# Kernel optimization log

Hardware: AMD Instinct MI355X
Metric: run time of the kernel (lower is better)

## Reference

```python
import jax, jax.numpy as jnp
import numpy as np

B, L, H, D, EF = 2, 2048, 16, 64, 4
HID = H * D            # 1024
QKVP = HID * (3 + EF)  # 7168
VP = HID * (1 + EF)    # 5120
LN_EPS = 1e-5


def layer_norm(x, g, b):
    m = jnp.mean(x, axis=-1, keepdims=True)
    v = jnp.mean(jnp.square(x - m), axis=-1, keepdims=True)
    return (x - m) * jax.lax.rsqrt(v + LN_EPS) * g + b


def shift_seq(x, n):
    # shift along seq (axis -2) by n, zero-padding the front (matches F.pad (0,0,n,-n))
    return jnp.pad(x, ((0, 0), (n, 0), (0, 0)))[:, :-n, :]


def setup_inputs() -> dict:
    key = jax.random.key(0)
    ks = jax.random.split(key, 4)
    x = jax.random.normal(ks[0], (B, L, HID), dtype=jnp.float32)
    W_in = jax.random.normal(ks[1], (QKVP, HID), dtype=jnp.float32) * (HID ** -0.5)
    W_out = jax.random.normal(ks[2], (HID, VP), dtype=jnp.float32) * (VP ** -0.5)
    slopes = (2.0 ** jnp.linspace(0.0, -6.0, H)).astype(jnp.float32)
    return {
        "x": x,
        "in_ln_g": jnp.ones((HID,), jnp.float32),
        "in_ln_b": jnp.zeros((HID,), jnp.float32),
        "W_in": W_in,
        "mid_ln_g": jnp.ones((QKVP,), jnp.float32),
        "mid_ln_b": jnp.zeros((QKVP,), jnp.float32),
        "slopes": slopes,
        "W_out": W_out,
        "out_ln_g": jnp.ones((HID,), jnp.float32),
        "out_ln_b": jnp.zeros((HID,), jnp.float32),
    }


def reference(x, in_ln_g, in_ln_b, W_in, mid_ln_g, mid_ln_b, slopes, W_out, out_ln_g, out_ln_b):
    b, l, d = x.shape
    d8 = d // 8
    x = layer_norm(x, in_ln_g, in_ln_b)
    # in-place torch shifts compose: ch [0,d/8) shifted by 1; ch [d/8,d/4) shifted by 1 then 2 (=3)
    x = jnp.concatenate([
        shift_seq(x[..., :d8], 1),
        shift_seq(x[..., d8:2 * d8], 3),
        x[..., 2 * d8:],
    ], axis=-1)
    h = layer_norm(jax.nn.relu(jnp.einsum('bld,od->blo', x, W_in)), mid_ln_g, mid_ln_b)
    q = h[..., :HID].reshape(b, l, H, D)
    k = h[..., HID:2 * HID].reshape(b, l, H, D)
    v = h[..., 2 * HID:3 * HID].reshape(b, l, H, D)
    p = h[..., 3 * HID:]  # [b, l, HID*EF]
    scores = jnp.einsum('bihd,bjhd->bhij', q, k) * (D ** -0.5)
    causal = jnp.where(jnp.tril(jnp.ones((l, l), dtype=bool)), 0.0, -1e10).astype(scores.dtype)
    alibi = jnp.arange(l, dtype=scores.dtype)[None, None, None, :] * slopes[None, :, None, None]
    a = jax.nn.softmax(scores + causal[None, None] + alibi, axis=-1)
    o = jnp.einsum('bhij,bjhd->bihd', a, v).reshape(b, l, HID)
    pg = jax.nn.gelu(p, approximate=False) * jnp.roll(p, 1, axis=-1)
    out = jnp.einsum('blv,dv->bld', jnp.concatenate([o, pg], axis=-1), W_out)
    return layer_norm(out, out_ln_g, out_ln_b)
```

## Files before the change

### kernel.cpp

```cpp
#include <hip/hip_runtime.h>
#include <math.h>

#define L_SEQ 2048
#define NB 2
#define NH 16
#define HID 1024
#define QKVP 7168
#define VP 5120
#define NROWS 4096
#define LN_EPS 1e-5f

typedef unsigned short u16;
using s16x4 = __attribute__((ext_vector_type(4))) short;
using s16x8 = __attribute__((ext_vector_type(8))) short;
using f32x4 = __attribute__((ext_vector_type(4))) float;

__device__ __forceinline__ u16 f2bf(float f) {
  unsigned u = __float_as_uint(f);
  u += 0x7FFFu + ((u >> 16) & 1u);
  return (u16)(u >> 16);
}
__device__ __forceinline__ float bf2f(u16 h) {
  return __uint_as_float((unsigned)h << 16);
}
struct HiLo { short hi, lo; };
__device__ __forceinline__ HiLo split2(float x) {
  HiLo r;
  const u16 h = f2bf(x);
  r.hi = (short)h;
  r.lo = (short)f2bf(x - bf2f(h));
  return r;
}
__device__ __forceinline__ void split4(float4 v, s16x4& h4, s16x4& l4) {
  const HiLo a = split2(v.x), b = split2(v.y), c = split2(v.z), d = split2(v.w);
  h4[0] = a.hi; l4[0] = a.lo;
  h4[1] = b.hi; l4[1] = b.lo;
  h4[2] = c.hi; l4[2] = c.lo;
  h4[3] = d.hi; l4[3] = d.lo;
}
__device__ __forceinline__ void split4v(f32x4 v, s16x4& h4, s16x4& l4) {
  const HiLo a = split2(v[0]), b = split2(v[1]), c = split2(v[2]), d = split2(v[3]);
  h4[0] = a.hi; l4[0] = a.lo;
  h4[1] = b.hi; l4[1] = b.lo;
  h4[2] = c.hi; l4[2] = c.lo;
  h4[3] = d.hi; l4[3] = d.lo;
}
__device__ __forceinline__ s16x8 shuf8(s16x4 a, s16x4 b) {
  return __builtin_shufflevector(a, b, 0, 1, 2, 3, 4, 5, 6, 7);
}

__device__ __forceinline__ float blk_sum256(float v, float* sm) {
#pragma unroll
  for (int m = 32; m >= 1; m >>= 1) v += __shfl_xor(v, m, 64);
  __syncthreads();
  if ((threadIdx.x & 63) == 0) sm[threadIdx.x >> 6] = v;
  __syncthreads();
  return sm[0] + sm[1] + sm[2] + sm[3];
}

__global__ __launch_bounds__(256) void ln_shift_kernel(
    const float* __restrict__ x, const float* __restrict__ g,
    const float* __restrict__ bb, float* __restrict__ xs) {
  __shared__ float sm[4];
  const int row = blockIdx.x;
  const int l = row & (L_SEQ - 1);
  const int t = threadIdx.x;
  const float4 v = reinterpret_cast<const float4*>(x + (size_t)row * HID)[t];
  float s = v.x + v.y + v.z + v.w;
  const float mean = blk_sum256(s, sm) * (1.0f / HID);
  const float dx = v.x - mean, dy = v.y - mean, dz = v.z - mean, dw = v.w - mean;
  const float sq = dx * dx + dy * dy + dz * dz + dw * dw;
  const float var = blk_sum256(sq, sm) * (1.0f / HID);
  const float rstd = rsqrtf(var + LN_EPS);
  const float4 gv = reinterpret_cast<const float4*>(g)[t];
  const float4 bv = reinterpret_cast<const float4*>(bb)[t];
  float4 n;
  n.x = dx * rstd * gv.x + bv.x;
  n.y = dy * rstd * gv.y + bv.y;
  n.z = dz * rstd * gv.z + bv.z;
  n.w = dw * rstd * gv.w + bv.w;
  const int c0 = t * 4;
  const float4 zero = make_float4(0.f, 0.f, 0.f, 0.f);
  if (c0 < 128) {
    if (l + 1 < L_SEQ) reinterpret_cast<float4*>(xs + (size_t)(row + 1) * HID)[t] = n;
    if (l == 0)        reinterpret_cast<float4*>(xs + (size_t)row * HID)[t] = zero;
  } else if (c0 < 256) {
    if (l + 3 < L_SEQ) reinterpret_cast<float4*>(xs + (size_t)(row + 3) * HID)[t] = n;
    if (l < 3)         reinterpret_cast<float4*>(xs + (size_t)row * HID)[t] = zero;
  } else {
    reinterpret_cast<float4*>(xs + (size_t)row * HID)[t] = n;
  }
}

template <bool RELU, bool A_REMAP>
__global__ __launch_bounds__(256, 2) void gemm_f32_hilo(
    const float* __restrict__ A, const float* __restrict__ Bw,
    float* __restrict__ C, int N, int K, int lda, int nbx) {
  __shared__ __align__(16) u16 Ah[128][40];
  __shared__ __align__(16) u16 Al[128][40];
  __shared__ __align__(16) u16 Bh[128][40];
  __shared__ __align__(16) u16 Bl[128][40];

  const int cpx = (int)gridDim.x >> 3;
  const int b0 = blockIdx.x;
  const int swz = (b0 & 7) * cpx + (b0 >> 3);
  const int bx = swz % nbx, by = swz / nbx;
  const int m0 = by * 128, n0 = bx * 128;

  const int t = threadIdx.x;
  const int lane = t & 63, w = t >> 6;
  const int wr = (w >> 1) * 64, wc = (w & 1) * 64;
  const int lrow = lane & 15;
  const int lkg = (lane >> 4) * 4;

  f32x4 acc[4][4] = {};

  const int sr = t >> 1;
  const int sk = (t & 1) * 16;

  for (int k0 = 0; k0 < K; k0 += 32) {
    int ak = sk + k0;
    if (A_REMAP && ak >= 1024) ak += 2048;
    const float* ap = A + (size_t)(m0 + sr) * lda + ak;
    const float* bp = Bw + (size_t)(n0 + sr) * K + sk + k0;
    const float4 av0 = *(const float4*)(ap);
    const float4 av1 = *(const float4*)(ap + 4);
    const float4 av2 = *(const float4*)(ap + 8);
    const float4 av3 = *(const float4*)(ap + 12);
    const float4 bv0 = *(const float4*)(bp);
    const float4 bv1 = *(const float4*)(bp + 4);
    const float4 bv2 = *(const float4*)(bp + 8);
    const float4 bv3 = *(const float4*)(bp + 12);
    __syncthreads();
    {
      s16x4 h0, l0, h1, l1;
      split4(av0, h0, l0); split4(av1, h1, l1);
      *(s16x8*)&Ah[sr][sk] = shuf8(h0, h1);
      *(s16x8*)&Al[sr][sk] = shuf8(l0, l1);
      split4(av2, h0, l0); split4(av3, h1, l1);
      *(s16x8*)&Ah[sr][sk + 8] = shuf8(h0, h1);
      *(s16x8*)&Al[sr][sk + 8] = shuf8(l0, l1);
      split4(bv0, h0, l0); split4(bv1, h1, l1);
      *(s16x8*)&Bh[sr][sk] = shuf8(h0, h1);
      *(s16x8*)&Bl[sr][sk] = shuf8(l0, l1);
      split4(bv2, h0, l0); split4(bv3, h1, l1);
      *(s16x8*)&Bh[sr][sk + 8] = shuf8(h0, h1);
      *(s16x8*)&Bl[sr][sk + 8] = shuf8(l0, l1);
    }
    __syncthreads();

    s16x8 afh[4], afl[4], bfh[4], bfl[4];
#pragma unroll
    for (int f = 0; f < 4; ++f) {
      const int ar = wr + f * 16 + lrow;
      const int bc = wc + f * 16 + lrow;
      s16x4 p0, p1;
      p0 = *(const s16x4*)&Ah[ar][lkg]; p1 = *(const s16x4*)&Ah[ar][16 + lkg];
      afh[f] = shuf8(p0, p1);
      p0 = *(const s16x4*)&Al[ar][lkg]; p1 = *(const s16x4*)&Al[ar][16 + lkg];
      afl[f] = shuf8(p0, p1);
      p0 = *(const s16x4*)&Bh[bc][lkg]; p1 = *(const s16x4*)&Bh[bc][16 + lkg];
      bfh[f] = shuf8(p0, p1);
      p0 = *(const s16x4*)&Bl[bc][lkg]; p1 = *(const s16x4*)&Bl[bc][16 + lkg];
      bfl[f] = shuf8(p0, p1);
    }
#pragma unroll
    for (int i = 0; i < 4; ++i)
#pragma unroll
      for (int j = 0; j < 4; ++j) {
        acc[i][j] = __builtin_amdgcn_mfma_f32_16x16x32_bf16(afh[i], bfh[j], acc[i][j], 0, 0, 0);
        acc[i][j] = __builtin_amdgcn_mfma_f32_16x16x32_bf16(afh[i], bfl[j], acc[i][j], 0, 0, 0);
        acc[i][j] = __builtin_amdgcn_mfma_f32_16x16x32_bf16(afl[i], bfh[j], acc[i][j], 0, 0, 0);
      }
  }
#pragma unroll
  for (int i = 0; i < 4; ++i) {
    const int row0 = m0 + wr + i * 16 + lkg;
#pragma unroll
    for (int j = 0; j < 4; ++j) {
      const int col = n0 + wc + j * 16 + lrow;
#pragma unroll
      for (int r = 0; r < 4; ++r) {
        float v = acc[i][j][r];
        if (RELU) v = fmaxf(v, 0.f);
        C[(size_t)(row0 + r) * N + col] = v;
      }
    }
  }
}

__global__ __launch_bounds__(256) void mid_ln_kernel(
    float* __restrict__ h, const float* __restrict__ g, const float* __restrict__ bb) {
  __shared__ float sm[4];
  const int row = blockIdx.x;
  const int t = threadIdx.x;
  float* hr = h + (size_t)row * QKVP;
  float4 r[7];
  float s = 0.f;
#pragma unroll
  for (int j = 0; j < 7; ++j) {
    r[j] = reinterpret_cast<float4*>(hr)[t + j * 256];
    s += r[j].x + r[j].y + r[j].z + r[j].w;
  }
  const float mean = blk_sum256(s, sm) * (1.0f / QKVP);
  float sq = 0.f;
#pragma unroll
  for (int j = 0; j < 7; ++j) {
    r[j].x -= mean; r[j].y -= mean; r[j].z -= mean; r[j].w -= mean;
    sq += r[j].x * r[j].x + r[j].y * r[j].y + r[j].z * r[j].z + r[j].w * r[j].w;
  }
  const float rstd = rsqrtf(blk_sum256(sq, sm) * (1.0f / QKVP) + LN_EPS);
#pragma unroll
  for (int j = 0; j < 7; ++j) {
    const float4 gv = reinterpret_cast<const float4*>(g)[t + j * 256];
    const float4 bv = reinterpret_cast<const float4*>(bb)[t + j * 256];
    float4 o;
    o.x = r[j].x * rstd * gv.x + bv.x;
    o.y = r[j].y * rstd * gv.y + bv.y;
    o.z = r[j].z * rstd * gv.z + bv.z;
    o.w = r[j].w * rstd * gv.w + bv.w;
    reinterpret_cast<float4*>(hr)[t + j * 256] = o;
  }
}

__global__ __launch_bounds__(256) void attn_kernel(
    float* __restrict__ h, const float* __restrict__ slopes) {
  __shared__ __align__(16) u16 Kh[64][72];
  __shared__ __align__(16) u16 Kl[64][72];
  __shared__ __align__(16) u16 Vh[64][76];
  __shared__ __align__(16) u16 Vl[64][76];
  const int it = blockIdx.x, bh = blockIdx.y;
  const int b = bh >> 4, hh = bh & 15;
  const float slope = slopes[hh];
  const int t = threadIdx.x;
  const int lane = t & 63, w = t >> 6;
  const int li = lane & 15;
  const int g = lane >> 4;
  const int i0 = it * 64;
  const size_t base = (size_t)b * L_SEQ * QKVP;
  const int myrow = i0 + w * 16 + li;

  s16x8 qh[2], ql[2];
  {
    const float* qp = h + base + (size_t)myrow * QKVP + hh * 64 + 8 * g;
#pragma unroll
    for (int ks = 0; ks < 2; ++ks) {
      const float4 a0 = *(const float4*)(qp + 32 * ks);
      const float4 a1 = *(const float4*)(qp + 32 * ks + 4);
      s16x4 h0, l0, h1, l1;
      split4(a0, h0, l0);
      split4(a1, h1, l1);
      qh[ks] = shuf8(h0, h1);
      ql[ks] = shuf8(l0, l1);
    }
  }

  float m_run = -INFINITY, l_run = 0.f;
  f32x4 ot[4] = {};

  const int sj = t >> 2, sd = (t & 3) * 16;
  const int vj = (t >> 4) * 4, vd = (t & 15) * 4;
  const float* kbase = h + base + HID + hh * 64;
  const float* vbase = h + base + 2 * HID + hh * 64;

  for (int jt = 0; jt <= it; ++jt) {
    const int j0 = jt * 64;
    float4 kq[4], vq[4];
#pragma unroll
    for (int q = 0; q < 4; ++q)
      kq[q] = *(const float4*)(kbase + (size_t)(j0 + sj) * QKVP + sd + 4 * q);
#pragma unroll
    for (int r = 0; r < 4; ++r)
      vq[r] = *(const float4*)(vbase + (size_t)(j0 + vj + r) * QKVP + vd);
    __syncthreads();
    {
      s16x4 h0, l0, h1, l1;
      split4(kq[0], h0, l0); split4(kq[1], h1, l1);
      *(s16x8*)&Kh[sj][sd] = shuf8(h0, h1);
      *(s16x8*)&Kl[sj][sd] = shuf8(l0, l1);
      split4(kq[2], h0, l0); split4(kq[3], h1, l1);
      *(s16x8*)&Kh[sj][sd + 8] = shuf8(h0, h1);
      *(s16x8*)&Kl[sj][sd + 8] = shuf8(l0, l1);
    }
    {
      s16x4 vh4[4], vl4[4];
#pragma unroll
      for (int r = 0; r < 4; ++r) split4(vq[r], vh4[r], vl4[r]);
#pragma unroll
      for (int c = 0; c < 4; ++c) {
        s16x4 hc, lc;
#pragma unroll
        for (int r = 0; r < 4; ++r) { hc[r] = vh4[r][c]; lc[r] = vl4[r][c]; }
        *(s16x4*)&Vh[vd + c][vj] = hc;
        *(s16x4*)&Vl[vd + c][vj] = lc;
      }
    }
    __syncthreads();

    f32x4 sa[4] = {};
#pragma unroll
    for (int j4 = 0; j4 < 4; ++j4) {
      const int jr = j4 * 16 + li;
#pragma unroll
      for (int ks = 0; ks < 2; ++ks) {
        const s16x8 kh = *(const s16x8*)&Kh[jr][ks * 32 + 8 * g];
        const s16x8 kl = *(const s16x8*)&Kl[jr][ks * 32 + 8 * g];
        sa[j4] = __builtin_amdgcn_mfma_f32_16x16x32_bf16(kh, qh[ks], sa[j4], 0, 0, 0);
        sa[j4] = __builtin_amdgcn_mfma_f32_16x16x32_bf16(kh, ql[ks], sa[j4], 0, 0, 0);
        sa[j4] = __builtin_amdgcn_mfma_f32_16x16x32_bf16(kl, qh[ks], sa[j4], 0, 0, 0);
      }
    }
    float pmax = -INFINITY;
#pragma unroll
    for (int j4 = 0; j4 < 4; ++j4)
#pragma unroll
      for (int r = 0; r < 4; ++r) {
        const int jg = j0 + j4 * 16 + 4 * g + r;
        float v = sa[j4][r] * 0.125f + (float)jg * slope;
        if (jg > myrow) v = -1e10f;
        sa[j4][r] = v;
        pmax = fmaxf(pmax, v);
      }
    pmax = fmaxf(pmax, __shfl_xor(pmax, 16));
    pmax = fmaxf(pmax, __shfl_xor(pmax, 32));
    const float m_new = fmaxf(m_run, pmax);
    const float corr = __expf(m_run - m_new);
    m_run = m_new;
    float ls = 0.f;
    s16x8 ph[2], pl[2];
#pragma unroll
    for (int ks = 0; ks < 2; ++ks) {
      f32x4 p0, p1;
#pragma unroll
      for (int r = 0; r < 4; ++r) {
        p0[r] = __expf(sa[2 * ks][r] - m_new);
        p1[r] = __expf(sa[2 * ks + 1][r] - m_new);
        ls += p0[r] + p1[r];
      }
      s16x4 h0, l0, h1, l1;
      split4v(p0, h0, l0);
      split4v(p1, h1, l1);
      ph[ks] = shuf8(h0, h1);
      pl[ks] = shuf8(l0, l1);
    }
    ls += __shfl_xor(ls, 16);
    ls += __shfl_xor(ls, 32);
    l_run = l_run * corr + ls;
#pragma unroll
    for (int dt = 0; dt < 4; ++dt)
#pragma unroll
      for (int r = 0; r < 4; ++r) ot[dt][r] *= corr;
#pragma unroll
    for (int dt = 0; dt < 4; ++dt) {
      const int dr = dt * 16 + li;
#pragma unroll
      for (int ks = 0; ks < 2; ++ks) {
        const s16x8 vh8 = shuf8(*(const s16x4*)&Vh[dr][ks * 32 + 4 * g],
                                *(const s16x4*)&Vh[dr][ks * 32 + 16 + 4 * g]);
        const s16x8 vl8 = shuf8(*(const s16x4*)&Vl[dr][ks * 32 + 4 * g],
                                *(const s16x4*)&Vl[dr][ks * 32 + 16 + 4 * g]);
        ot[dt] = __builtin_amdgcn_mfma_f32_16x16x32_bf16(vh8, ph[ks], ot[dt], 0, 0, 0);
        ot[dt] = __builtin_amdgcn_mfma_f32_16x16x32_bf16(vh8, pl[ks], ot[dt], 0, 0, 0);
        ot[dt] = __builtin_amdgcn_mfma_f32_16x16x32_bf16(vl8, ph[ks], ot[dt], 0, 0, 0);
      }
    }
  }
  const float inv = 1.0f / l_run;
  float* op = h + base + (size_t)myrow * QKVP + hh * 64;
#pragma unroll
  for (int dt = 0; dt < 4; ++dt) {
    float4 ov;
    ov.x = ot[dt][0] * inv;
    ov.y = ot[dt][1] * inv;
    ov.z = ot[dt][2] * inv;
    ov.w = ot[dt][3] * inv;
    *(float4*)(op + dt * 16 + 4 * g) = ov;
  }
}

__device__ __forceinline__ float gelu_exact(float x) {
  return 0.5f * x * (1.0f + erff(x * 0.70710678118654752f));
}
__global__ __launch_bounds__(256) void pg_kernel(float* __restrict__ h) {
  const int row = blockIdx.x;
  float* p = h + (size_t)row * QKVP + 3 * HID;
  const int t = threadIdx.x;
  float4 v[4];
  float pm1[4];
#pragma unroll
  for (int j = 0; j < 4; ++j) {
    const int c4 = t + j * 256;
    v[j] = reinterpret_cast<float4*>(p)[c4];
    pm1[j] = p[(c4 * 4 - 1) & 4095];
  }
  __syncthreads();
#pragma unroll
  for (int j = 0; j < 4; ++j) {
    const int c4 = t + j * 256;
    float4 o;
    o.x = gelu_exact(v[j].x) * pm1[j];
    o.y = gelu_exact(v[j].y) * v[j].x;
    o.z = gelu_exact(v[j].z) * v[j].y;
    o.w = gelu_exact(v[j].w) * v[j].z;
    reinterpret_cast<float4*>(p)[c4] = o;
  }
}

__global__ __launch_bounds__(256) void ln1024_kernel(
    float* __restrict__ io, const float* __restrict__ g, const float* __restrict__ bb) {
  __shared__ float sm[4];
  const int row = blockIdx.x;
  const int t = threadIdx.x;
  float* xr = io + (size_t)row * HID;
  const float4 v = reinterpret_cast<const float4*>(xr)[t];
  float s = v.x + v.y + v.z + v.w;
  const float mean = blk_sum256(s, sm) * (1.0f / HID);
  const float dx = v.x - mean, dy = v.y - mean, dz = v.z - mean, dw = v.w - mean;
  const float sq = dx * dx + dy * dy + dz * dz + dw * dw;
  const float var = blk_sum256(sq, sm) * (1.0f / HID);
  const float rstd = rsqrtf(var + LN_EPS);
  const float4 gv = reinterpret_cast<const float4*>(g)[t];
  const float4 bv = reinterpret_cast<const float4*>(bb)[t];
  float4 n;
  n.x = dx * rstd * gv.x + bv.x;
  n.y = dy * rstd * gv.y + bv.y;
  n.z = dz * rstd * gv.z + bv.z;
  n.w = dw * rstd * gv.w + bv.w;
  reinterpret_cast<float4*>(xr)[t] = n;
}

extern "C" void kernel_launch(void* const* d_in, const int* in_sizes, int n_in,
                              void* d_out, int out_size, void* d_ws, size_t ws_size,
                              hipStream_t stream) {
  const float* x      = (const float*)d_in[0];
  const float* in_g   = (const float*)d_in[1];
  const float* in_b   = (const float*)d_in[2];
  const float* W_in   = (const float*)d_in[3];
  const float* mid_g  = (const float*)d_in[4];
  const float* mid_b  = (const float*)d_in[5];
  const float* slopes = (const float*)d_in[6];
  const float* W_out  = (const float*)d_in[7];
  const float* out_g  = (const float*)d_in[8];
  const float* out_b  = (const float*)d_in[9];
  float* out = (float*)d_out;

  float* h  = (float*)d_ws;
  float* xs = out;
  const size_t needed = (size_t)NROWS * QKVP * sizeof(float);
  if (ws_size < needed) return;

  ln_shift_kernel<<<NROWS, 256, 0, stream>>>(x, in_g, in_b, xs);
  gemm_f32_hilo<true, false><<<(NROWS / 128) * (QKVP / 128), 256, 0, stream>>>(
      xs, W_in, h, QKVP, HID, HID, QKVP / 128);
  mid_ln_kernel<<<NROWS, 256, 0, stream>>>(h, mid_g, mid_b);
  attn_kernel<<<dim3(L_SEQ / 64, NB * NH), 256, 0, stream>>>(h, slopes);
  pg_kernel<<<NROWS, 256, 0, stream>>>(h);
  gemm_f32_hilo<false, true><<<(NROWS / 128) * (HID / 128), 256, 0, stream>>>(
      h, W_out, out, HID, VP, QKVP, HID / 128);
  ln1024_kernel<<<NROWS, 256, 0, stream>>>(out, out_g, out_b);
}
```

Baseline: 961.3 us.

## Store activations as pre-split bf16 hi/lo planes across the pipeline

Every producer kernel (input LN+shift, the first GEMM epilogue, mid LN, attention, pg) now writes activations as separate bf16 hi and lo arrays instead of fp32. Consumers load the split halves directly, so the repeated fp32-to-hi/lo splitting is removed. The GEMM now reads A fragments straight from global memory into registers, which drops the A tiles from shared memory, and its occupancy hint rises from 2 to 3. Re-splitting after mid LN round-trips through the hi+lo approximation, which may change rounding slightly. The direct A global loads are strided per lane and may coalesce less well.

```diff
diff --git a/kernel.cpp b/kernel.cpp
--- a/kernel.cpp
+++ b/kernel.cpp
@@ -48,6 +48,9 @@
 __device__ __forceinline__ s16x8 shuf8(s16x4 a, s16x4 b) {
   return __builtin_shufflevector(a, b, 0, 1, 2, 3, 4, 5, 6, 7);
 }
+__device__ __forceinline__ float rec2(s16x4 hv, s16x4 lv, int i) {
+  return bf2f((u16)hv[i]) + bf2f((u16)lv[i]);
+}
 
 __device__ __forceinline__ float blk_sum256(float v, float* sm) {
 #pragma unroll
@@ -60,7 +63,7 @@
 
 __global__ __launch_bounds__(256) void ln_shift_kernel(
     const float* __restrict__ x, const float* __restrict__ g,
-    const float* __restrict__ bb, float* __restrict__ xs) {
+    const float* __restrict__ bb, u16* __restrict__ xh, u16* __restrict__ xl) {
   __shared__ float sm[4];
   const int row = blockIdx.x;
   const int l = row & (L_SEQ - 1);
@@ -79,25 +82,40 @@
   n.y = dy * rstd * gv.y + bv.y;
   n.z = dz * rstd * gv.z + bv.z;
   n.w = dw * rstd * gv.w + bv.w;
+  s16x4 h4, l4;
+  split4(n, h4, l4);
+  const s16x4 z4 = {0, 0, 0, 0};
   const int c0 = t * 4;
-  const float4 zero = make_float4(0.f, 0.f, 0.f, 0.f);
   if (c0 < 128) {
-    if (l + 1 < L_SEQ) reinterpret_cast<float4*>(xs + (size_t)(row + 1) * HID)[t] = n;
-    if (l == 0)        reinterpret_cast<float4*>(xs + (size_t)row * HID)[t] = zero;
+    if (l + 1 < L_SEQ) {
+      *(s16x4*)(xh + (size_t)(row + 1) * HID + c0) = h4;
+      *(s16x4*)(xl + (size_t)(row + 1) * HID + c0) = l4;
+    }
+    if (l == 0) {
+      *(s16x4*)(xh + (size_t)row * HID + c0) = z4;
+      *(s16x4*)(xl + (size_t)row * HID + c0) = z4;
+    }
   } else if (c0 < 256) {
-    if (l + 3 < L_SEQ) reinterpret_cast<float4*>(xs + (size_t)(row + 3) * HID)[t] = n;
-    if (l < 3)         reinterpret_cast<float4*>(xs + (size_t)row * HID)[t] = zero;
+    if (l + 3 < L_SEQ) {
+      *(s16x4*)(xh + (size_t)(row + 3) * HID + c0) = h4;
+      *(s16x4*)(xl + (size_t)(row + 3) * HID + c0) = l4;
+    }
+    if (l < 3) {
+      *(s16x4*)(xh + (size_t)row * HID + c0) = z4;
+      *(s16x4*)(xl + (size_t)row * HID + c0) = z4;
+    }
   } else {
-    reinterpret_cast<float4*>(xs + (size_t)row * HID)[t] = n;
-  }
-}
-
-template <bool RELU, bool A_REMAP>
-__global__ __launch_bounds__(256, 2) void gemm_f32_hilo(
-    const float* __restrict__ A, const float* __restrict__ Bw,
-    float* __restrict__ C, int N, int K, int lda, int nbx) {
-  __shared__ __align__(16) u16 Ah[128][40];
-  __shared__ __align__(16) u16 Al[128][40];
+    *(s16x4*)(xh + (size_t)row * HID + c0) = h4;
+    *(s16x4*)(xl + (size_t)row * HID + c0) = l4;
+  }
+}
+
+template <bool RELU, bool A_REMAP, bool SPLIT_OUT>
+__global__ __launch_bounds__(256, 3) void gemm_asplit(
+    const u16* __restrict__ Ahi, const u16* __restrict__ Alo,
+    const float* __restrict__ Bw, float* __restrict__ C,
+    u16* __restrict__ Chi, u16* __restrict__ Clo,
+    int N, int K, int lda, int nbx) {
   __shared__ __align__(16) u16 Bh[128][40];
   __shared__ __align__(16) u16 Bl[128][40];
 
@@ -110,36 +128,36 @@
   const int t = threadIdx.x;
   const int lane = t & 63, w = t >> 6;
   const int wr = (w >> 1) * 64, wc = (w & 1) * 64;
-  const int lrow = lane & 15;
-  const int lkg = (lane >> 4) * 4;
+  const int li = lane & 15;
+  const int g = lane >> 4;
 
   f32x4 acc[4][4] = {};
 
   const int sr = t >> 1;
   const int sk = (t & 1) * 16;
 
+  size_t arow[4];
+#pragma unroll
+  for (int f = 0; f < 4; ++f)
+    arow[f] = (size_t)(m0 + wr + f * 16 + li) * lda;
+
   for (int k0 = 0; k0 < K; k0 += 32) {
-    int ak = sk + k0;
-    if (A_REMAP && ak >= 1024) ak += 2048;
-    const float* ap = A + (size_t)(m0 + sr) * lda + ak;
     const float* bp = Bw + (size_t)(n0 + sr) * K + sk + k0;
-    const float4 av0 = *(const float4*)(ap);
-    const float4 av1 = *(const float4*)(ap + 4);
-    const float4 av2 = *(const float4*)(ap + 8);
-    const float4 av3 = *(const float4*)(ap + 12);
     const float4 bv0 = *(const float4*)(bp);
     const float4 bv1 = *(const float4*)(bp + 4);
     const float4 bv2 = *(const float4*)(bp + 8);
     const float4 bv3 = *(const float4*)(bp + 12);
+    int ak = k0 + 8 * g;
+    if (A_REMAP && ak >= 1024) ak += 2048;
+    s16x8 afh[4], afl[4];
+#pragma unroll
+    for (int f = 0; f < 4; ++f) {
+      afh[f] = *(const s16x8*)(Ahi + arow[f] + ak);
+      afl[f] = *(const s16x8*)(Alo + arow[f] + ak);
+    }
     __syncthreads();
     {
       s16x4 h0, l0, h1, l1;
-      split4(av0, h0, l0); split4(av1, h1, l1);
-      *(s16x8*)&Ah[sr][sk] = shuf8(h0, h1);
-      *(s16x8*)&Al[sr][sk] = shuf8(l0, l1);
-      split4(av2, h0, l0); split4(av3, h1, l1);
-      *(s16x8*)&Ah[sr][sk + 8] = shuf8(h0, h1);
-      *(s16x8*)&Al[sr][sk + 8] = shuf8(l0, l1);
       split4(bv0, h0, l0); split4(bv1, h1, l1);
       *(s16x8*)&Bh[sr][sk] = shuf8(h0, h1);
       *(s16x8*)&Bl[sr][sk] = shuf8(l0, l1);
@@ -149,20 +167,11 @@
     }
     __syncthreads();
 
-    s16x8 afh[4], afl[4], bfh[4], bfl[4];
+    s16x8 bfh[4], bfl[4];
 #pragma unroll
     for (int f = 0; f < 4; ++f) {
-      const int ar = wr + f * 16 + lrow;
-      const int bc = wc + f * 16 + lrow;
-      s16x4 p0, p1;
-      p0 = *(const s16x4*)&Ah[ar][lkg]; p1 = *(const s16x4*)&Ah[ar][16 + lkg];
-      afh[f] = shuf8(p0, p1);
-      p0 = *(const s16x4*)&Al[ar][lkg]; p1 = *(const s16x4*)&Al[ar][16 + lkg];
-      afl[f] = shuf8(p0, p1);
-      p0 = *(const s16x4*)&Bh[bc][lkg]; p1 = *(const s16x4*)&Bh[bc][16 + lkg];
-      bfh[f] = shuf8(p0, p1);
-      p0 = *(const s16x4*)&Bl[bc][lkg]; p1 = *(const s16x4*)&Bl[bc][16 + lkg];
-      bfl[f] = shuf8(p0, p1);
+      bfh[f] = *(const s16x8*)&Bh[wc + f * 16 + li][8 * g];
+      bfl[f] = *(const s16x8*)&Bl[wc + f * 16 + li][8 * g];
     }
 #pragma unroll
     for (int i = 0; i < 4; ++i)
@@ -175,31 +184,46 @@
   }
 #pragma unroll
   for (int i = 0; i < 4; ++i) {
-    const int row0 = m0 + wr + i * 16 + lkg;
+    const int row0 = m0 + wr + i * 16 + 4 * g;
 #pragma unroll
     for (int j = 0; j < 4; ++j) {
-      const int col = n0 + wc + j * 16 + lrow;
+      const int col = n0 + wc + j * 16 + li;
 #pragma unroll
       for (int r = 0; r < 4; ++r) {
         float v = acc[i][j][r];
         if (RELU) v = fmaxf(v, 0.f);
-        C[(size_t)(row0 + r) * N + col] = v;
+        const size_t off = (size_t)(row0 + r) * N + col;
+        if constexpr (SPLIT_OUT) {
+          const HiLo sp = split2(v);
+          Chi[off] = (u16)sp.hi;
+          Clo[off] = (u16)sp.lo;
+        } else {
+          C[off] = v;
+        }
       }
     }
   }
 }
 
 __global__ __launch_bounds__(256) void mid_ln_kernel(
-    float* __restrict__ h, const float* __restrict__ g, const float* __restrict__ bb) {
+    u16* __restrict__ hh_, u16* __restrict__ hl_,
+    const float* __restrict__ g, const float* __restrict__ bb) {
   __shared__ float sm[4];
   const int row = blockIdx.x;
   const int t = threadIdx.x;
-  float* hr = h + (size_t)row * QKVP;
+  u16* hr = hh_ + (size_t)row * QKVP;
+  u16* lr = hl_ + (size_t)row * QKVP;
   float4 r[7];
   float s = 0.f;
 #pragma unroll
   for (int j = 0; j < 7; ++j) {
-    r[j] = reinterpret_cast<float4*>(hr)[t + j * 256];
+    const int c = 4 * t + j * 1024;
+    const s16x4 hv = *(const s16x4*)(hr + c);
+    const s16x4 lv = *(const s16x4*)(lr + c);
+    r[j].x = rec2(hv, lv, 0);
+    r[j].y = rec2(hv, lv, 1);
+    r[j].z = rec2(hv, lv, 2);
+    r[j].w = rec2(hv, lv, 3);
     s += r[j].x + r[j].y + r[j].z + r[j].w;
   }
   const float mean = blk_sum256(s, sm) * (1.0f / QKVP);
@@ -212,19 +236,24 @@
   const float rstd = rsqrtf(blk_sum256(sq, sm) * (1.0f / QKVP) + LN_EPS);
 #pragma unroll
   for (int j = 0; j < 7; ++j) {
-    const float4 gv = reinterpret_cast<const float4*>(g)[t + j * 256];
-    const float4 bv = reinterpret_cast<const float4*>(bb)[t + j * 256];
+    const int c = 4 * t + j * 1024;
+    const float4 gv = *(const float4*)(g + c);
+    const float4 bv = *(const float4*)(bb + c);
     float4 o;
     o.x = r[j].x * rstd * gv.x + bv.x;
     o.y = r[j].y * rstd * gv.y + bv.y;
     o.z = r[j].z * rstd * gv.z + bv.z;
     o.w = r[j].w * rstd * gv.w + bv.w;
-    reinterpret_cast<float4*>(hr)[t + j * 256] = o;
+    s16x4 h4, l4;
+    split4(o, h4, l4);
+    *(s16x4*)(hr + c) = h4;
+    *(s16x4*)(lr + c) = l4;
   }
 }
 
 __global__ __launch_bounds__(256) void attn_kernel(
-    float* __restrict__ h, const float* __restrict__ slopes) {
+    u16* __restrict__ hh_, u16* __restrict__ hl_,
+    const float* __restrict__ slopes) {
   __shared__ __align__(16) u16 Kh[64][72];
   __shared__ __align__(16) u16 Kl[64][72];
   __shared__ __align__(16) u16 Vh[64][76];
@@ -242,16 +271,12 @@
 
   s16x8 qh[2], ql[2];
   {
-    const float* qp = h + base + (size_t)myrow * QKVP + hh * 64 + 8 * g;
+    const u16* qph = hh_ + base + (size_t)myrow * QKVP + hh * 64 + 8 * g;
+    const u16* qpl = hl_ + base + (size_t)myrow * QKVP + hh * 64 + 8 * g;
 #pragma unroll
     for (int ks = 0; ks < 2; ++ks) {
-      const float4 a0 = *(const float4*)(qp + 32 * ks);
-      const float4 a1 = *(const float4*)(qp + 32 * ks + 4);
-      s16x4 h0, l0, h1, l1;
-      split4(a0, h0, l0);
-      split4(a1, h1, l1);
-      qh[ks] = shuf8(h0, h1);
-      ql[ks] = shuf8(l0, l1);
+      qh[ks] = *(const s16x8*)(qph + 32 * ks);
+      ql[ks] = *(const s16x8*)(qpl + 32 * ks);
     }
   }
 
@@ -260,40 +285,37 @@
 
   const int sj = t >> 2, sd = (t & 3) * 16;
   const int vj = (t >> 4) * 4, vd = (t & 15) * 4;
-  const float* kbase = h + base + HID + hh * 64;
-  const float* vbase = h + base + 2 * HID + hh * 64;
+  const u16* kbh = hh_ + base + HID + hh * 64;
+  const u16* kbl = hl_ + base + HID + hh * 64;
+  const u16* vbh = hh_ + base + 2 * HID + hh * 64;
+  const u16* vbl = hl_ + base + 2 * HID + hh * 64;
 
   for (int jt = 0; jt <= it; ++jt) {
     const int j0 = jt * 64;
-    float4 kq[4], vq[4];
-#pragma unroll
-    for (int q = 0; q < 4; ++q)
-      kq[q] = *(const float4*)(kbase + (size_t)(j0 + sj) * QKVP + sd + 4 * q);
-#pragma unroll
-    for (int r = 0; r < 4; ++r)
-      vq[r] = *(const float4*)(vbase + (size_t)(j0 + vj + r) * QKVP + vd);
+    const size_t ko = (size_t)(j0 + sj) * QKVP + sd;
+    const s16x8 k0h = *(const s16x8*)(kbh + ko);
+    const s16x8 k1h = *(const s16x8*)(kbh + ko + 8);
+    const s16x8 k0l = *(const s16x8*)(kbl + ko);
+    const s16x8 k1l = *(const s16x8*)(kbl + ko + 8);
+    s16x4 vh4[4], vl4[4];
+#pragma unroll
+    for (int r = 0; r < 4; ++r) {
+      const size_t vo = (size_t)(j0 + vj + r) * QKVP + vd;
+      vh4[r] = *(const s16x4*)(vbh + vo);
+      vl4[r] = *(const s16x4*)(vbl + vo);
+    }
     __syncthreads();
-    {
-      s16x4 h0, l0, h1, l1;
-      split4(kq[0], h0, l0); split4(kq[1], h1, l1);
-      *(s16x8*)&Kh[sj][sd] = shuf8(h0, h1);
-      *(s16x8*)&Kl[sj][sd] = shuf8(l0, l1);
-      split4(kq[2], h0, l0); split4(kq[3], h1, l1);
-      *(s16x8*)&Kh[sj][sd + 8] = shuf8(h0, h1);
-      *(s16x8*)&Kl[sj][sd + 8] = shuf8(l0, l1);
-    }
-    {
-      s16x4 vh4[4], vl4[4];
-#pragma unroll
-      for (int r = 0; r < 4; ++r) split4(vq[r], vh4[r], vl4[r]);
-#pragma unroll
-      for (int c = 0; c < 4; ++c) {
-        s16x4 hc, lc;
-#pragma unroll
-        for (int r = 0; r < 4; ++r) { hc[r] = vh4[r][c]; lc[r] = vl4[r][c]; }
-        *(s16x4*)&Vh[vd + c][vj] = hc;
-        *(s16x4*)&Vl[vd + c][vj] = lc;
-      }
+    *(s16x8*)&Kh[sj][sd] = k0h;
+    *(s16x8*)&Kh[sj][sd + 8] = k1h;
+    *(s16x8*)&Kl[sj][sd] = k0l;
+    *(s16x8*)&Kl[sj][sd + 8] = k1l;
+#pragma unroll
+    for (int c = 0; c < 4; ++c) {
+      s16x4 hc, lc;
+#pragma unroll
+      for (int r = 0; r < 4; ++r) { hc[r] = vh4[r][c]; lc[r] = vl4[r][c]; }
+      *(s16x4*)&Vh[vd + c][vj] = hc;
+      *(s16x4*)&Vl[vd + c][vj] = lc;
     }
     __syncthreads();
 
@@ -366,43 +388,58 @@
     }
   }
   const float inv = 1.0f / l_run;
-  float* op = h + base + (size_t)myrow * QKVP + hh * 64;
+  u16* oph = hh_ + base + (size_t)myrow * QKVP + hh * 64;
+  u16* opl = hl_ + base + (size_t)myrow * QKVP + hh * 64;
 #pragma unroll
   for (int dt = 0; dt < 4; ++dt) {
-    float4 ov;
-    ov.x = ot[dt][0] * inv;
-    ov.y = ot[dt][1] * inv;
-    ov.z = ot[dt][2] * inv;
-    ov.w = ot[dt][3] * inv;
-    *(float4*)(op + dt * 16 + 4 * g) = ov;
+    f32x4 ov;
+    ov[0] = ot[dt][0] * inv;
+    ov[1] = ot[dt][1] * inv;
+    ov[2] = ot[dt][2] * inv;
+    ov[3] = ot[dt][3] * inv;
+    s16x4 h4, l4;
+    split4v(ov, h4, l4);
+    *(s16x4*)(oph + dt * 16 + 4 * g) = h4;
+    *(s16x4*)(opl + dt * 16 + 4 * g) = l4;
   }
 }
 
 __device__ __forceinline__ float gelu_exact(float x) {
   return 0.5f * x * (1.0f + erff(x * 0.70710678118654752f));
 }
-__global__ __launch_bounds__(256) void pg_kernel(float* __restrict__ h) {
+__global__ __launch_bounds__(256) void pg_kernel(
+    u16* __restrict__ hh_, u16* __restrict__ hl_) {
   const int row = blockIdx.x;
-  float* p = h + (size_t)row * QKVP + 3 * HID;
+  u16* ph = hh_ + (size_t)row * QKVP + 3 * HID;
+  u16* pl = hl_ + (size_t)row * QKVP + 3 * HID;
   const int t = threadIdx.x;
   float4 v[4];
   float pm1[4];
 #pragma unroll
   for (int j = 0; j < 4; ++j) {
-    const int c4 = t + j * 256;
-    v[j] = reinterpret_cast<float4*>(p)[c4];
-    pm1[j] = p[(c4 * 4 - 1) & 4095];
+    const int c0 = 4 * (t + j * 256);
+    const s16x4 hv = *(const s16x4*)(ph + c0);
+    const s16x4 lv = *(const s16x4*)(pl + c0);
+    v[j].x = rec2(hv, lv, 0);
+    v[j].y = rec2(hv, lv, 1);
+    v[j].z = rec2(hv, lv, 2);
+    v[j].w = rec2(hv, lv, 3);
+    const int cm = (c0 - 1) & 4095;
+    pm1[j] = bf2f(ph[cm]) + bf2f(pl[cm]);
   }
   __syncthreads();
 #pragma unroll
   for (int j = 0; j < 4; ++j) {
-    const int c4 = t + j * 256;
+    const int c0 = 4 * (t + j * 256);
     float4 o;
     o.x = gelu_exact(v[j].x) * pm1[j];
     o.y = gelu_exact(v[j].y) * v[j].x;
     o.z = gelu_exact(v[j].z) * v[j].y;
     o.w = gelu_exact(v[j].w) * v[j].z;
-    reinterpret_cast<float4*>(p)[c4] = o;
+    s16x4 h4, l4;
+    split4(o, h4, l4);
+    *(s16x4*)(ph + c0) = h4;
+    *(s16x4*)(pl + c0) = l4;
   }
 }
 
@@ -444,18 +481,20 @@
   const float* out_b  = (const float*)d_in[9];
   float* out = (float*)d_out;
 
-  float* h  = (float*)d_ws;
-  float* xs = out;
-  const size_t needed = (size_t)NROWS * QKVP * sizeof(float);
+  u16* h_hi = (u16*)d_ws;
+  u16* h_lo = h_hi + (size_t)NROWS * QKVP;
+  u16* xs_hi = (u16*)out;
+  u16* xs_lo = xs_hi + (size_t)NROWS * HID;
+  const size_t needed = (size_t)NROWS * QKVP * 4;
   if (ws_size < needed) return;
 
-  ln_shift_kernel<<<NROWS, 256, 0, stream>>>(x, in_g, in_b, xs);
-  gemm_f32_hilo<true, false><<<(NROWS / 128) * (QKVP / 128), 256, 0, stream>>>(
-      xs, W_in, h, QKVP, HID, HID, QKVP / 128);
-  mid_ln_kernel<<<NROWS, 256, 0, stream>>>(h, mid_g, mid_b);
-  attn_kernel<<<dim3(L_SEQ / 64, NB * NH), 256, 0, stream>>>(h, slopes);
-  pg_kernel<<<NROWS, 256, 0, stream>>>(h);
-  gemm_f32_hilo<false, true><<<(NROWS / 128) * (HID / 128), 256, 0, stream>>>(
-      h, W_out, out, HID, VP, QKVP, HID / 128);
+  ln_shift_kernel<<<NROWS, 256, 0, stream>>>(x, in_g, in_b, xs_hi, xs_lo);
+  gemm_asplit<true, false, true><<<(NROWS / 128) * (QKVP / 128), 256, 0, stream>>>(
+      xs_hi, xs_lo, W_in, nullptr, h_hi, h_lo, QKVP, HID, HID, QKVP / 128);
+  mid_ln_kernel<<<NROWS, 256, 0, stream>>>(h_hi, h_lo, mid_g, mid_b);
+  attn_kernel<<<dim3(L_SEQ / 64, NB * NH), 256, 0, stream>>>(h_hi, h_lo, slopes);
+  pg_kernel<<<NROWS, 256, 0, stream>>>(h_hi, h_lo);
+  gemm_asplit<false, true, false><<<(NROWS / 128) * (HID / 128), 256, 0, stream>>>(
+      h_hi, h_lo, W_out, out, nullptr, nullptr, HID, VP, QKVP, HID / 128);
   ln1024_kernel<<<NROWS, 256, 0, stream>>>(out, out_g, out_b);
 }
```

Result: faster. 897.4 us (-6.6%).
